# Kernel optimization log

Measured on AMD Instinct MI355X. Metric: run time of the kernel, lower is better.

The kernel has to match this reference:

```python
import jax, jax.numpy as jnp
import numpy as np

EPS_DIST = 1e-7  # matches torch: log((d+1)/(d+1e-7))


def _cdist(x, p):
    # x: (B, N, D), p: (P, D) -> (B, N, P) Euclidean distances
    x2 = jnp.sum(x * x, axis=-1, keepdims=True)        # (B, N, 1)
    p2 = jnp.sum(p * p, axis=-1)                       # (P,)
    d2 = x2 + p2[None, None, :] - 2.0 * jnp.einsum('bnd,pd->bnp', x, p)
    return jnp.sqrt(jnp.maximum(d2, 1e-12))


def setup_inputs() -> dict:
    key = jax.random.key(0)
    k1, k2, k3 = jax.random.split(key, 3)
    B, C, H, W = 32, 2048, 14, 14
    num_classes, npc = 200, 10
    P = num_classes * npc
    x = jax.random.normal(k1, (B, C, H, W), dtype=jnp.float32)
    prototypes = jax.random.normal(k2, (1, P, C), dtype=jnp.float32)
    fc_w = jax.random.normal(k3, (num_classes, P), dtype=jnp.float32) * 0.02
    return {"x": x, "prototypes": prototypes, "fc_w": fc_w}


def reference(x, prototypes, fc_w):
    B, C, H, W = x.shape
    feats = x.reshape(B, C, H * W).transpose(0, 2, 1)   # (B, HW, D)
    protos = prototypes[0]                              # (P, D)
    num_classes = fc_w.shape[0]
    npc = protos.shape[0] // num_classes

    distances = _cdist(feats, protos)                   # (B, HW, P)
    similarity = jnp.log((distances + 1.0) / (distances + EPS_DIST))
    max_similarity = jnp.max(similarity, axis=1)        # (B, P)
    min_distances = jnp.min(distances, axis=1)          # (B, P)
    min_distances_per_class = min_distances.reshape(B, num_classes, npc)
    scores = max_similarity @ fc_w.T                    # (B, num_classes)
    return scores, min_distances_per_class
```

## Files before the change

kernel.cpp:

```cpp
#include <hip/hip_runtime.h>

#define INF_BITS 0x7F800000u
#define AS1 __attribute__((address_space(1)))
#define AS3 __attribute__((address_space(3)))

typedef float f32x4 __attribute__((ext_vector_type(4)));
typedef unsigned int u32x2 __attribute__((ext_vector_type(2)));
typedef unsigned int u32x4 __attribute__((ext_vector_type(4)));

template <int SEL>
static __device__ __forceinline__ float dq8(unsigned int w) {
  return __builtin_amdgcn_cvt_f32_fp8((int)w, SEL);
}

__global__ __launch_bounds__(256) void k_prep_p(const float* __restrict__ protos,
                                                unsigned char* __restrict__ pTf,
                                                float* __restrict__ p2,
                                                unsigned int* __restrict__ outu) {
  const int row = blockIdx.x;
  const int tid = threadIdx.x;
  const int gi = row * 256 + tid;
  if (gi < 64000) outu[6400 + gi] = INF_BITS;
  __shared__ float red[4];
  float s = 0.f;
  unsigned int w0 = 0u, w1 = 0u;
  if (row < 2000) {
    const float* src = protos + (size_t)row * 2048 + tid * 8;
    f32x4 a = *(const f32x4*)src;
    f32x4 c = *(const f32x4*)(src + 4);
    w0 = (unsigned int)__builtin_amdgcn_cvt_pk_fp8_f32(a.x, a.y, 0, false);
    w0 = (unsigned int)__builtin_amdgcn_cvt_pk_fp8_f32(a.z, a.w, (int)w0, true);
    w1 = (unsigned int)__builtin_amdgcn_cvt_pk_fp8_f32(c.x, c.y, 0, false);
    w1 = (unsigned int)__builtin_amdgcn_cvt_pk_fp8_f32(c.z, c.w, (int)w1, true);
    float q;
    q = dq8<0>(w0); s += q * q;
    q = dq8<1>(w0); s += q * q;
    q = dq8<2>(w0); s += q * q;
    q = dq8<3>(w0); s += q * q;
    q = dq8<0>(w1); s += q * q;
    q = dq8<1>(w1); s += q * q;
    q = dq8<2>(w1); s += q * q;
    q = dq8<3>(w1); s += q * q;
  }
  *(u32x2*)(pTf + (size_t)row * 2048 + tid * 8) = (u32x2){w0, w1};
  #pragma unroll
  for (int off = 32; off; off >>= 1) s += __shfl_xor(s, off);
  if ((tid & 63) == 0) red[tid >> 6] = s;
  __syncthreads();
  if (tid == 0) p2[row] = red[0] + red[1] + red[2] + red[3];
}

__global__ __launch_bounds__(256) void k_prep_x(const float* __restrict__ x,
                                                unsigned char* __restrict__ xTf,
                                                float* __restrict__ x2p,
                                                float* __restrict__ x2) {
  const int kt = blockIdx.x;
  const int b  = blockIdx.y;
  const int tid = threadIdx.x;
  if (b == 32) {
    u32x4* pad = (u32x4*)(xTf + (size_t)6272 * 2048);
    #pragma unroll
    for (int j = tid; j < 512; j += 256)
      pad[kt * 512 + j] = (u32x4){0u, 0u, 0u, 0u};
    if (kt == 0 && tid < 128) x2[6272 + tid] = __uint_as_float(INF_BITS);
    return;
  }
  __shared__ unsigned char Ls[64][208];
  const float* src = x + ((size_t)b * 2048 + (size_t)kt * 64) * 196;
  for (int idx = tid; idx < 3136; idx += 256) {
    const int kk = idx / 49, c4 = idx - kk * 49;
    f32x4 v = *(const f32x4*)(src + (size_t)kk * 196 + c4 * 4);
    unsigned int w = (unsigned int)__builtin_amdgcn_cvt_pk_fp8_f32(v.x, v.y, 0, false);
    w = (unsigned int)__builtin_amdgcn_cvt_pk_fp8_f32(v.z, v.w, (int)w, true);
    *(unsigned int*)&Ls[kk][c4 * 4] = w;
  }
  __syncthreads();
  if (tid < 196) {
    float s = 0.f;
    #pragma unroll
    for (int j = 0; j < 64; ++j) {
      float v = dq8<0>((unsigned int)Ls[j][tid]);
      s += v * v;
    }
    x2p[kt * 6272 + b * 196 + tid] = s;
  }
  unsigned char* dstb = xTf + (size_t)b * 196 * 2048 + kt * 64;
  for (int idx = tid; idx < 784; idx += 256) {
    const int n = idx >> 2, q = idx & 3;
    const int k0 = q * 16;
    u32x4 v;
    #pragma unroll
    for (int j = 0; j < 4; ++j) {
      v[j] = (unsigned int)Ls[k0 + 4 * j + 0][n] |
             ((unsigned int)Ls[k0 + 4 * j + 1][n] << 8) |
             ((unsigned int)Ls[k0 + 4 * j + 2][n] << 16) |
             ((unsigned int)Ls[k0 + 4 * j + 3][n] << 24);
    }
    *(u32x4*)(dstb + (size_t)n * 2048 + k0) = v;
  }
}

__global__ void k_x2r(const float* __restrict__ x2p, float* __restrict__ x2) {
  int i = blockIdx.x * blockDim.x + threadIdx.x;
  if (i >= 6272) return;
  float s = 0.f;
  #pragma unroll
  for (int c = 0; c < 32; ++c) s += x2p[c * 6272 + i];
  x2[i] = s;
}

__global__ __launch_bounds__(512, 2) void k_main(
    const unsigned char* __restrict__ pTf, const unsigned char* __restrict__ xTf,
    const float* __restrict__ p2, const float* __restrict__ x2,
    unsigned int* __restrict__ outu) {
  const int orig = blockIdx.x;
  const int wgid = (orig & 7) * 25 + (orig >> 3);
  const int ptpair = wgid / 50;
  const int rem = wgid - ptpair * 50;
  const int ptile = ptpair * 2 + (rem & 1);
  const int mtile = rem >> 1;
  const int p0 = ptile * 256;
  const int m0 = mtile * 256;
  const int tid = threadIdx.x;
  const int lane = tid & 63;
  const int w = tid >> 6;
  const int wp = w >> 2;
  const int wn = w & 3;
  const int lr = lane & 15;
  const int lg = lane >> 4;

  __shared__ __align__(16) char S[131072];

  f32x4 acc[8][4];
  #pragma unroll
  for (int mi = 0; mi < 8; ++mi)
    #pragma unroll
    for (int ni = 0; ni < 4; ++ni)
      acc[mi][ni] = (f32x4){0.f, 0.f, 0.f, 0.f};

  const int rowbase = tid >> 3;
  const int chunk = (tid & 7) ^ (rowbase & 7);
  const char* gA = (const char*)pTf + (size_t)(p0 + rowbase) * 2048 + chunk * 16;
  const char* gB = (const char*)xTf + (size_t)(m0 + rowbase) * 2048 + chunk * 16;
  const int wbase = w * 1024;

#define STAGE_A(c_, kt_, h_) do {                                              \
    const char* s_ = gA + (size_t)((h_) * 128 * 2048) + (size_t)(kt_) * 128;   \
    _Pragma("unroll")                                                          \
    for (int j_ = 0; j_ < 2; ++j_)                                             \
      __builtin_amdgcn_global_load_lds(                                        \
          (const AS1 void*)(s_ + (size_t)j_ * 64 * 2048),                      \
          (AS3 void*)(S + (c_) * 32768 + (h_) * 16384 + j_ * 8192 + wbase),    \
          16, 0, 0);                                                           \
  } while (0)
#define STAGE_B(c_, kt_, h_) do {                                              \
    const char* s_ = gB + (size_t)((h_) * 128 * 2048) + (size_t)(kt_) * 128;   \
    _Pragma("unroll")                                                          \
    for (int j_ = 0; j_ < 2; ++j_)                                             \
      __builtin_amdgcn_global_load_lds(                                        \
          (const AS1 void*)(s_ + (size_t)j_ * 64 * 2048),                      \
          (AS3 void*)(S + 65536 + (c_) * 32768 + (h_) * 16384 + j_ * 8192 + wbase), \
          16, 0, 0);                                                           \
  } while (0)

  const int arow = (wp * 128 + lr) * 128;
  const int brow = (wn * 64 + lr) * 128;
  int koff[4];
  #pragma unroll
  for (int ks = 0; ks < 4; ++ks)
    koff[ks] = (((2 * ks + (lg >> 1)) ^ (lr & 7)) << 4) | ((lg & 1) << 3);

#define READ_A(dst_, c_, hf_, kp_)                                             \
    _Pragma("unroll")                                                          \
    for (int ks_ = 0; ks_ < 2; ++ks_)                                          \
      _Pragma("unroll")                                                        \
      for (int mi_ = 0; mi_ < 4; ++mi_)                                        \
        dst_[ks_ * 4 + mi_] = *(const long*)(S + (c_) * 32768 + arow +         \
            ((hf_) * 4 + mi_) * 2048 + koff[(kp_) * 2 + ks_]);
#define READ_B(dst_, c_, kp_)                                                  \
    _Pragma("unroll")                                                          \
    for (int ks_ = 0; ks_ < 2; ++ks_)                                          \
      _Pragma("unroll")                                                        \
      for (int ni_ = 0; ni_ < 4; ++ni_)                                        \
        dst_[ks_ * 4 + ni_] = *(const long*)(S + 65536 + (c_) * 32768 + brow + \
            ni_ * 2048 + koff[(kp_) * 2 + ks_]);

#define PH_BAR() do { __builtin_amdgcn_sched_barrier(0);                       \
    __builtin_amdgcn_s_barrier(); __builtin_amdgcn_sched_barrier(0); } while (0)
#define LGKM0() do { asm volatile("s_waitcnt lgkmcnt(0)" ::: "memory");        \
    __builtin_amdgcn_sched_barrier(0); } while (0)
#define MFMA_Q(mlo_, af_, bf_) do { __builtin_amdgcn_s_setprio(1);             \
    _Pragma("unroll")                                                          \
    for (int ks_ = 0; ks_ < 2; ++ks_)                                          \
      _Pragma("unroll")                                                        \
      for (int mi_ = 0; mi_ < 4; ++mi_)                                        \
        _Pragma("unroll")                                                      \
        for (int ni_ = 0; ni_ < 4; ++ni_)                                      \
          acc[(mlo_) + mi_][ni_] = __builtin_amdgcn_mfma_f32_16x16x32_fp8_fp8( \
              af_[ks_ * 4 + mi_], bf_[ks_ * 4 + ni_], acc[(mlo_) + mi_][ni_],  \
              0, 0, 0);                                                        \
    __builtin_amdgcn_s_setprio(0); } while (0)

#define KT_BODY(kt_, c_, sa_, sb_, vm_) do {                                   \
    long alo[8], ahi[8], b01[8], b23[8];                                       \
    READ_A(alo, c_, 0, 0);                                                     \
    READ_B(b01, c_, 0);                                                        \
    if (sa_) STAGE_A((c_) ^ 1, (kt_) + 1, 0);                                  \
    PH_BAR(); LGKM0();                                                         \
    MFMA_Q(0, alo, b01);                                                       \
    PH_BAR();                                                                  \
    READ_A(ahi, c_, 1, 0);                                                     \
    READ_B(b23, c_, 1);                                                        \
    if (sa_) STAGE_A((c_) ^ 1, (kt_) + 1, 1);                                  \
    PH_BAR(); LGKM0();                                                         \
    MFMA_Q(4, ahi, b01);                                                       \
    PH_BAR();                                                                  \
    READ_A(alo, c_, 0, 1);                                                     \
    if (sb_) STAGE_B(c_, (kt_) + 2, 0);                                        \
    PH_BAR(); LGKM0();                                                         \
    MFMA_Q(0, alo, b23);                                                       \
    PH_BAR();                                                                  \
    READ_A(ahi, c_, 1, 1);                                                     \
    if (sb_) STAGE_B(c_, (kt_) + 2, 1);                                        \
    if ((vm_) == 4)      asm volatile("s_waitcnt vmcnt(4)" ::: "memory");      \
    else if ((vm_) == 0) asm volatile("s_waitcnt vmcnt(0)" ::: "memory");      \
    __builtin_amdgcn_sched_barrier(0);                                         \
    PH_BAR(); LGKM0();                                                         \
    MFMA_Q(4, ahi, b23);                                                       \
    PH_BAR();                                                                  \
  } while (0)

  STAGE_B(0, 0, 0); STAGE_B(0, 0, 1);
  STAGE_A(0, 0, 0); STAGE_A(0, 0, 1);
  STAGE_B(1, 1, 0); STAGE_B(1, 1, 1);
  asm volatile("s_waitcnt vmcnt(4)" ::: "memory");
  __builtin_amdgcn_sched_barrier(0);
  __builtin_amdgcn_s_barrier();
  __builtin_amdgcn_sched_barrier(0);

  #pragma unroll 1
  for (int it = 0; it < 7; ++it) {
    KT_BODY(2 * it, 0, 1, 1, 4);
    KT_BODY(2 * it + 1, 1, 1, 1, 4);
  }
  KT_BODY(14, 0, 1, 0, 0);
  KT_BODY(15, 1, 0, 0, -1);
#undef KT_BODY
#undef MFMA_Q
#undef READ_A
#undef READ_B
#undef STAGE_A
#undef STAGE_B

  const int wm_base = m0 + wn * 64;
  const int b_lo = wm_base / 196;
  int b_hi = (wm_base + 63) / 196;
  if (b_hi > 31) b_hi = 31;
  const bool wave_ok = (b_lo < 32);
  float x2v[4];
  int seg0[4];
  #pragma unroll
  for (int ni = 0; ni < 4; ++ni) {
    const int m = wm_base + ni * 16 + lr;
    x2v[ni] = x2[m];
    seg0[ni] = ((m / 196) == b_lo);
  }
  const float INF = __uint_as_float(INF_BITS);
  #pragma unroll
  for (int mi = 0; mi < 8; ++mi) {
    const int prow = p0 + wp * 128 + mi * 16 + 4 * lg;
    #pragma unroll
    for (int j = 0; j < 4; ++j) {
      const int p = prow + j;
      const float pp = p2[p];
      float ma = INF, mb = INF;
      #pragma unroll
      for (int ni = 0; ni < 4; ++ni) {
        const float d2 = x2v[ni] + pp - 2.f * acc[mi][ni][j];
        ma = fminf(ma, seg0[ni] ? d2 : INF);
        mb = fminf(mb, seg0[ni] ? INF : d2);
      }
      #pragma unroll
      for (int off = 1; off < 16; off <<= 1) {
        ma = fminf(ma, __shfl_xor(ma, off));
        mb = fminf(mb, __shfl_xor(mb, off));
      }
      if (lr == 0 && p < 2000 && wave_ok) {
        atomicMin(&outu[6400 + b_lo * 2000 + p], __float_as_uint(fmaxf(ma, 0.f)));
        if (b_hi != b_lo)
          atomicMin(&outu[6400 + b_hi * 2000 + p], __float_as_uint(fmaxf(mb, 0.f)));
      }
    }
  }
}

__global__ void k_post(float* __restrict__ out, float* __restrict__ simbuf) {
  int i = blockIdx.x * blockDim.x + threadIdx.x;
  if (i >= 64000) return;
  float d2 = out[6400 + i];
  float d = sqrtf(fmaxf(d2, 1e-12f));
  out[6400 + i] = d;
  simbuf[i] = logf((d + 1.0f) / (d + 1e-7f));
}

__global__ __launch_bounds__(256) void k_scores(const float* __restrict__ fc_w,
                                                const float* __restrict__ simbuf,
                                                float* __restrict__ out) {
  const int id = blockIdx.x * 4 + (threadIdx.x >> 6);
  const int lane = threadIdx.x & 63;
  const int b = id / 200;
  const int c = id - b * 200;
  const f32x4* sv = (const f32x4*)(simbuf + (size_t)b * 2000);
  const f32x4* wv = (const f32x4*)(fc_w + (size_t)c * 2000);
  float s = 0.f;
  #pragma unroll
  for (int it = 0; it < 8; ++it) {
    int i = lane + it * 64;
    if (i < 500) {
      f32x4 a = sv[i], w4 = wv[i];
      s += a.x * w4.x + a.y * w4.y + a.z * w4.z + a.w * w4.w;
    }
  }
  #pragma unroll
  for (int off = 32; off; off >>= 1) s += __shfl_xor(s, off);
  if (lane == 0) out[b * 200 + c] = s;
}

extern "C" void kernel_launch(void* const* d_in, const int* in_sizes, int n_in,
                              void* d_out, int out_size, void* d_ws, size_t ws_size,
                              hipStream_t stream) {
  const float* x      = (const float*)d_in[0];
  const float* protos = (const float*)d_in[1];
  const float* fc_w   = (const float*)d_in[2];
  float* out = (float*)d_out;

  char* wsb = (char*)d_ws;
  unsigned char* pTf = (unsigned char*)wsb;
  unsigned char* xTf = (unsigned char*)(wsb + 4194304);
  float* p2   = (float*)(wsb + 17301504);
  float* x2   = (float*)(wsb + 17309696);
  float* x2p  = (float*)(wsb + 17335296);
  float* simb = (float*)(wsb + 17335296);

  k_prep_p<<<2048, 256, 0, stream>>>(protos, pTf, p2, (unsigned int*)d_out);
  k_prep_x<<<dim3(32, 33), 256, 0, stream>>>(x, xTf, x2p, x2);
  k_x2r<<<25, 256, 0, stream>>>(x2p, x2);
  k_main<<<200, 512, 0, stream>>>(pTf, xTf, p2, x2, (unsigned int*)d_out);
  k_post<<<250, 256, 0, stream>>>(out, simb);
  k_scores<<<1600, 256, 0, stream>>>(fc_w, simb, out);
}
```

Measured before the change: 99.84 us.

## Switch FP8 GEMM to 16x16x128 scaled MFMA with wider LDS reads

Replaces the 16x16x32 fp8 MFMA with the gfx950 scaled 16x16x128 f8f6f4 MFMA. Each instruction now covers a whole 128-wide K slice, with unit scales. Operands are read from LDS as two 16-byte loads per row instead of many 8-byte loads. The per-K-tile schedule drops from four MFMA phases to two, and the A and B global-to-LDS staging calls are regrouped to match. This cuts MFMA issue count, LDS instruction count and barriers. The risks are a changed K ordering within the swizzled layout and higher register pressure from holding all of A and B at once.

```diff
diff --git a/kernel.cpp b/kernel.cpp
--- a/kernel.cpp
+++ b/kernel.cpp
@@ -5,6 +5,8 @@
 #define AS3 __attribute__((address_space(3)))
 
 typedef float f32x4 __attribute__((ext_vector_type(4)));
+typedef int i32x4 __attribute__((ext_vector_type(4)));
+typedef int i32x8 __attribute__((ext_vector_type(8)));
 typedef unsigned int u32x2 __attribute__((ext_vector_type(2)));
 typedef unsigned int u32x4 __attribute__((ext_vector_type(4)));
 
@@ -163,27 +165,29 @@
           16, 0, 0);                                                           \
   } while (0)
 
+  const int swz = ((lr & 7) << 4);
+  const int koffA = (lg * 32) ^ swz;
   const int arow = (wp * 128 + lr) * 128;
   const int brow = (wn * 64 + lr) * 128;
-  int koff[4];
-  #pragma unroll
-  for (int ks = 0; ks < 4; ++ks)
-    koff[ks] = (((2 * ks + (lg >> 1)) ^ (lr & 7)) << 4) | ((lg & 1) << 3);
-
-#define READ_A(dst_, c_, hf_, kp_)                                             \
-    _Pragma("unroll")                                                          \
-    for (int ks_ = 0; ks_ < 2; ++ks_)                                          \
-      _Pragma("unroll")                                                        \
-      for (int mi_ = 0; mi_ < 4; ++mi_)                                        \
-        dst_[ks_ * 4 + mi_] = *(const long*)(S + (c_) * 32768 + arow +         \
-            ((hf_) * 4 + mi_) * 2048 + koff[(kp_) * 2 + ks_]);
-#define READ_B(dst_, c_, kp_)                                                  \
-    _Pragma("unroll")                                                          \
-    for (int ks_ = 0; ks_ < 2; ++ks_)                                          \
-      _Pragma("unroll")                                                        \
-      for (int ni_ = 0; ni_ < 4; ++ni_)                                        \
-        dst_[ks_ * 4 + ni_] = *(const long*)(S + 65536 + (c_) * 32768 + brow + \
-            ni_ * 2048 + koff[(kp_) * 2 + ks_]);
+
+#define READ_A4(dst_, c_, hf_)                                                 \
+    _Pragma("unroll")                                                          \
+    for (int mi_ = 0; mi_ < 4; ++mi_) {                                        \
+      const char* p_ = S + (c_) * 32768 + arow + ((hf_) * 4 + mi_) * 2048;     \
+      u32x4 lo_ = *(const u32x4*)(p_ + koffA);                                 \
+      u32x4 hi_ = *(const u32x4*)(p_ + (koffA ^ 16));                          \
+      dst_[mi_] = __builtin_bit_cast(i32x8,                                    \
+          __builtin_shufflevector(lo_, hi_, 0, 1, 2, 3, 4, 5, 6, 7));          \
+    }
+#define READ_B4(dst_, c_)                                                      \
+    _Pragma("unroll")                                                          \
+    for (int ni_ = 0; ni_ < 4; ++ni_) {                                        \
+      const char* p_ = S + 65536 + (c_) * 32768 + brow + ni_ * 2048;           \
+      u32x4 lo_ = *(const u32x4*)(p_ + koffA);                                 \
+      u32x4 hi_ = *(const u32x4*)(p_ + (koffA ^ 16));                          \
+      dst_[ni_] = __builtin_bit_cast(i32x8,                                    \
+          __builtin_shufflevector(lo_, hi_, 0, 1, 2, 3, 4, 5, 6, 7));          \
+    }
 
 #define PH_BAR() do { __builtin_amdgcn_sched_barrier(0);                       \
     __builtin_amdgcn_s_barrier(); __builtin_amdgcn_sched_barrier(0); } while (0)
@@ -191,47 +195,35 @@
     __builtin_amdgcn_sched_barrier(0); } while (0)
 #define MFMA_Q(mlo_, af_, bf_) do { __builtin_amdgcn_s_setprio(1);             \
     _Pragma("unroll")                                                          \
-    for (int ks_ = 0; ks_ < 2; ++ks_)                                          \
+    for (int mi_ = 0; mi_ < 4; ++mi_)                                          \
       _Pragma("unroll")                                                        \
-      for (int mi_ = 0; mi_ < 4; ++mi_)                                        \
-        _Pragma("unroll")                                                      \
-        for (int ni_ = 0; ni_ < 4; ++ni_)                                      \
-          acc[(mlo_) + mi_][ni_] = __builtin_amdgcn_mfma_f32_16x16x32_fp8_fp8( \
-              af_[ks_ * 4 + mi_], bf_[ks_ * 4 + ni_], acc[(mlo_) + mi_][ni_],  \
-              0, 0, 0);                                                        \
+      for (int ni_ = 0; ni_ < 4; ++ni_)                                        \
+        acc[(mlo_) + mi_][ni_] =                                               \
+            __builtin_amdgcn_mfma_scale_f32_16x16x128_f8f6f4(                  \
+                af_[mi_], bf_[ni_], acc[(mlo_) + mi_][ni_],                    \
+                0, 0, 0, 0x7F7F7F7F, 0, 0x7F7F7F7F);                           \
     __builtin_amdgcn_s_setprio(0); } while (0)
 
 #define KT_BODY(kt_, c_, sa_, sb_, vm_) do {                                   \
-    long alo[8], ahi[8], b01[8], b23[8];                                       \
-    READ_A(alo, c_, 0, 0);                                                     \
-    READ_B(b01, c_, 0);                                                        \
-    if (sa_) STAGE_A((c_) ^ 1, (kt_) + 1, 0);                                  \
+    i32x8 af[4], bf[4];                                                        \
+    READ_B4(bf, c_);                                                           \
+    READ_A4(af, c_, 0);                                                        \
+    if (sa_) { STAGE_A((c_) ^ 1, (kt_) + 1, 0); STAGE_A((c_) ^ 1, (kt_) + 1, 1); } \
     PH_BAR(); LGKM0();                                                         \
-    MFMA_Q(0, alo, b01);                                                       \
+    MFMA_Q(0, af, bf);                                                         \
     PH_BAR();                                                                  \
-    READ_A(ahi, c_, 1, 0);                                                     \
-    READ_B(b23, c_, 1);                                                        \
-    if (sa_) STAGE_A((c_) ^ 1, (kt_) + 1, 1);                                  \
+    READ_A4(af, c_, 1);                                                        \
+    if (sb_) { STAGE_B(c_, (kt_) + 2, 0); STAGE_B(c_, (kt_) + 2, 1); }         \
     PH_BAR(); LGKM0();                                                         \
-    MFMA_Q(4, ahi, b01);                                                       \
-    PH_BAR();                                                                  \
-    READ_A(alo, c_, 0, 1);                                                     \
-    if (sb_) STAGE_B(c_, (kt_) + 2, 0);                                        \
-    PH_BAR(); LGKM0();                                                         \
-    MFMA_Q(0, alo, b23);                                                       \
-    PH_BAR();                                                                  \
-    READ_A(ahi, c_, 1, 1);                                                     \
-    if (sb_) STAGE_B(c_, (kt_) + 2, 1);                                        \
+    MFMA_Q(4, af, bf);                                                         \
     if ((vm_) == 4)      asm volatile("s_waitcnt vmcnt(4)" ::: "memory");      \
     else if ((vm_) == 0) asm volatile("s_waitcnt vmcnt(0)" ::: "memory");      \
     __builtin_amdgcn_sched_barrier(0);                                         \
-    PH_BAR(); LGKM0();                                                         \
-    MFMA_Q(4, ahi, b23);                                                       \
     PH_BAR();                                                                  \
   } while (0)
 
+  STAGE_A(0, 0, 0); STAGE_A(0, 0, 1);
   STAGE_B(0, 0, 0); STAGE_B(0, 0, 1);
-  STAGE_A(0, 0, 0); STAGE_A(0, 0, 1);
   STAGE_B(1, 1, 0); STAGE_B(1, 1, 1);
   asm volatile("s_waitcnt vmcnt(4)" ::: "memory");
   __builtin_amdgcn_sched_barrier(0);
@@ -247,8 +239,8 @@
   KT_BODY(15, 1, 0, 0, -1);
 #undef KT_BODY
 #undef MFMA_Q
-#undef READ_A
-#undef READ_B
+#undef READ_A4
+#undef READ_B4
 #undef STAGE_A
 #undef STAGE_B
 
```

Result: faster. 87.52 us (-12.3%).
